# Performance work log

Hardware: AMD Instinct MI355X
Metric: run time of the kernel (lower is better)

## Reference

```python
import jax, jax.numpy as jnp
import numpy as np
from jax import lax

BN_EPS = 1e-5


def _conv_bn_relu(x, W, b, gamma, beta):
    # x: [B, Cin, N]; W: [Cout, Cin]; 1x1 conv == channel GEMM
    y = jnp.einsum('oc,bcn->bon', W, x) + b[None, :, None]
    mean = jnp.mean(y, axis=(0, 2), keepdims=True)
    var = jnp.mean((y - mean) ** 2, axis=(0, 2), keepdims=True)  # biased, torch BN train mode
    y = gamma[None, :, None] * (y - mean) / jnp.sqrt(var + BN_EPS) + beta[None, :, None]
    return jax.nn.relu(y)


def setup_inputs() -> dict:
    key = jax.random.key(0)
    ks = jax.random.split(key, 8)
    B, N1, N2, C1, C2 = 16, 4096, 1024, 128, 256
    Cin, H = C1 + C2, 256  # MLP dims [384, 256, 256]
    inp = {
        'centroids1': jax.random.normal(ks[0], (B, 3, N1), jnp.float32),
        'centroids2': jax.random.normal(ks[1], (B, 3, N2), jnp.float32),
        'features1': jax.random.normal(ks[2], (B, C1, N1), jnp.float32),
        'features2': jax.random.normal(ks[3], (B, C2, N2), jnp.float32),
        'W1': jax.random.normal(ks[4], (H, Cin), jnp.float32) / np.sqrt(Cin),
        'b1': jnp.zeros((H,), jnp.float32),
        'g1': jnp.ones((H,), jnp.float32),
        'be1': jnp.zeros((H,), jnp.float32),
        'W2': jax.random.normal(ks[5], (H, H), jnp.float32) / np.sqrt(H),
        'b2': jnp.zeros((H,), jnp.float32),
        'g2': jnp.ones((H,), jnp.float32),
        'be2': jnp.zeros((H,), jnp.float32),
    }
    return inp


def reference(centroids1, centroids2, features1, features2,
              W1, b1, g1, be1, W2, b2, g2, be2):
    c1 = centroids1.transpose(0, 2, 1)  # [B, N1, 3]
    c2 = centroids2.transpose(0, 2, 1)  # [B, N2, 3]
    f2 = features2.transpose(0, 2, 1)   # [B, N2, C2]

    # pairwise squared distances [B, N1, N2]
    d = (jnp.sum(c1 ** 2, -1)[:, :, None] + jnp.sum(c2 ** 2, -1)[:, None, :]
         - 2.0 * jnp.einsum('bnd,bmd->bnm', c1, c2))

    # 3 nearest neighbors (smallest distances)
    neg_top, idx = lax.top_k(-d, 3)            # idx: [B, N1, 3]
    dist3 = -neg_top
    recip = 1.0 / (dist3 + 1e-8)
    weight = recip / jnp.sum(recip, axis=2, keepdims=True)  # [B, N1, 3]

    gathered = jax.vmap(lambda f, i: f[i])(f2, idx)         # [B, N1, 3, C2]
    interp = jnp.sum(gathered * weight[..., None], axis=2)  # [B, N1, C2]

    feats = jnp.concatenate((features1.transpose(0, 2, 1), interp), axis=-1)  # [B, N1, C1+C2]
    x = feats.transpose(0, 2, 1)  # [B, C1+C2, N1]
    x = _conv_bn_relu(x, W1, b1, g1, be1)
    x = _conv_bn_relu(x, W2, b2, g2, be2)
    return x  # [B, 256, N1]
```

## Files before the change

### kernel.cpp

```cpp
#include <hip/hip_runtime.h>
#include <math.h>

#define N1 4096
#define N2 1024
#define C1 128
#define C2 256
#define CIN 384
#define H 256
#define BATCH 16
#define BN_EPS 1e-5f

typedef __attribute__((ext_vector_type(8))) short bf16x8;
typedef __attribute__((ext_vector_type(4))) float f32x4;

__device__ inline float bf2f(short s) {
    union { unsigned u; float f; } x;
    x.u = ((unsigned)(unsigned short)s) << 16;
    return x.f;
}
__device__ inline short f2bf(float f) {
    union { float f; unsigned u; } x; x.f = f;
    unsigned r = x.u + 0x7fffu + ((x.u >> 16) & 1u);
    return (short)(r >> 16);
}

__global__ __launch_bounds__(256)
void knn_kernel(const float* __restrict__ c1, const float* __restrict__ c2,
                float4* __restrict__ pk) {
    __shared__ __align__(16) float4 sc[N2];
    __shared__ float md[64 * 13];
    __shared__ int   mi[64 * 13];
    const int b = blockIdx.y;
    const float* c2b = c2 + (size_t)b * 3 * N2;
    for (int j = threadIdx.x; j < N2; j += 256) {
        float xx = c2b[j], yy = c2b[N2 + j], zz = c2b[2 * N2 + j];
        sc[j] = make_float4(xx, yy, zz, xx * xx + yy * yy + zz * zz);
    }
    __syncthreads();

    const int t = threadIdx.x;
    const int q = t & 63;
    const int quarter = t >> 6;
    const int n = blockIdx.x * 64 + q;
    const float* c1b = c1 + (size_t)b * 3 * N1;
    const float x = c1b[n], y = c1b[N1 + n], z = c1b[2 * N1 + n];
    const float s1 = x * x + y * y + z * z;

    float d0 = 3.4e38f, d1 = 3.4e38f, d2 = 3.4e38f;
    int i0 = 0, i1 = 0, i2 = 0;
    const int j0 = quarter * 256;
    #pragma unroll 8
    for (int jj = 0; jj < 256; ++jj) {
        const int j = j0 + jj;
        float4 cc = sc[j];
        float dot = x * cc.x + y * cc.y + z * cc.z;
        float d = s1 + cc.w - 2.0f * dot;
        bool c0v = d < d0, c1v = d < d1, c2v = d < d2;
        i2 = c1v ? i1 : (c2v ? j : i2);
        i1 = c0v ? i0 : (c1v ? j : i1);
        i0 = c0v ? j  : i0;
        d2 = __builtin_amdgcn_fmed3f(d1, d2, d);
        d1 = __builtin_amdgcn_fmed3f(d0, d1, d);
        d0 = fminf(d0, d);
    }
    const int mb = q * 13 + quarter * 3;
    md[mb + 0] = d0; md[mb + 1] = d1; md[mb + 2] = d2;
    mi[mb + 0] = i0; mi[mb + 1] = i1; mi[mb + 2] = i2;
    __syncthreads();

    if (t < 64) {
        float e0 = 3.4e38f, e1 = 3.4e38f, e2 = 3.4e38f;
        int a0 = 0, a1 = 0, a2 = 0;
        #pragma unroll
        for (int r = 0; r < 12; ++r) {
            const int rr = t * 13 + (r / 3) * 3 + (r % 3);
            float d = md[rr]; int j = mi[rr];
            bool c0 = d < e0, c1v = d < e1, c2v = d < e2;
            e2 = c1v ? e1 : (c2v ? d : e2);  a2 = c1v ? a1 : (c2v ? j : a2);
            e1 = c0 ? e0 : (c1v ? d : e1);   a1 = c0 ? a0 : (c1v ? j : a1);
            e0 = c0 ? d  : e0;               a0 = c0 ? j  : a0;
        }
        float r0 = 1.0f / (e0 + 1e-8f);
        float r1 = 1.0f / (e1 + 1e-8f);
        float r2 = 1.0f / (e2 + 1e-8f);
        float rs = r0 + r1 + r2;
        unsigned pack = (unsigned)a0 | ((unsigned)a1 << 10) | ((unsigned)a2 << 20);
        pk[(size_t)b * N1 + n] = make_float4(__uint_as_float(pack), r0 / rs, r1 / rs, r2 / rs);
    }
}

__global__ __launch_bounds__(256)
void prep_w(const float* __restrict__ W, short* __restrict__ Wsw, int K) {
    const int nkb = K >> 3;
    const int id = blockIdx.x * 256 + threadIdx.x;
    if (id >= 256 * nkb) return;
    const int m = id / nkb, kb = id % nkb;
    const float* src = W + (size_t)m * K + kb * 8;
    bf16x8 v;
    #pragma unroll
    for (int j = 0; j < 8; ++j) v[j] = f2bf(src[j]);
    *(bf16x8*)(Wsw + ((size_t)kb * 256 + m) * 8) = v;
}

__global__ __launch_bounds__(256)
void transpose_f2(const float* __restrict__ f2, short* __restrict__ f2t) {
    __shared__ float st[32][33];
    const int j0 = blockIdx.x * 32, c0 = blockIdx.y * 32, b = blockIdx.z;
    const int t = threadIdx.x;
    {
        const int cc = t >> 3, jj = (t & 7) * 4;
        const float* src = f2 + ((size_t)b * C2 + c0 + cc) * N2 + j0 + jj;
        float4 v = *(const float4*)src;
        st[cc][jj + 0] = v.x; st[cc][jj + 1] = v.y;
        st[cc][jj + 2] = v.z; st[cc][jj + 3] = v.w;
    }
    __syncthreads();
    {
        const int j = t >> 3, cb = (t & 7) * 4;
        short4 v = { f2bf(st[cb + 0][j]), f2bf(st[cb + 1][j]),
                     f2bf(st[cb + 2][j]), f2bf(st[cb + 3][j]) };
        *(short4*)(f2t + ((size_t)b * N2 + j0 + j) * C2 + c0 + cb) = v;
    }
}

__global__ __launch_bounds__(256)
void prep_B1(const short* __restrict__ f2t, const float4* __restrict__ pk,
             short* __restrict__ B1) {
    const int b = blockIdx.y;
    const int n = blockIdx.x * 256 + threadIdx.x;
    float4 v = pk[(size_t)b * N1 + n];
    unsigned u = __float_as_uint(v.x);
    const short* r0 = f2t + ((size_t)b * N2 + (u & 1023u)) * C2;
    const short* r1 = f2t + ((size_t)b * N2 + ((u >> 10) & 1023u)) * C2;
    const short* r2 = f2t + ((size_t)b * N2 + ((u >> 20) & 1023u)) * C2;
    short* ob = B1 + ((size_t)b * 32 * N1 + n) * 8;
    #pragma unroll 4
    for (int kb = 0; kb < 32; ++kb) {
        bf16x8 g0 = *(const bf16x8*)(r0 + kb * 8);
        bf16x8 g1 = *(const bf16x8*)(r1 + kb * 8);
        bf16x8 g2 = *(const bf16x8*)(r2 + kb * 8);
        bf16x8 o;
        #pragma unroll
        for (int e = 0; e < 8; ++e)
            o[e] = f2bf(fmaf(v.w, bf2f(g2[e]), fmaf(v.z, bf2f(g1[e]), v.y * bf2f(g0[e]))));
        *(bf16x8*)(ob + (size_t)kb * N1 * 8) = o;
    }
}

template<int MODE>
__global__ __launch_bounds__(256, 4)
void gemm_kernel(const short* __restrict__ Wsw,
                 const float* __restrict__ f1, const short* __restrict__ Bkc,
                 const float* __restrict__ scale, const float* __restrict__ shift,
                 short* __restrict__ Ykc, float2* __restrict__ P) {
    __shared__ float sc_s[256], sh_s[256];
    __shared__ float2 pb[128][2];

    const int t = threadIdx.x;
    const int d = blockIdx.x;
    const int grp = d >> 4, rem = d & 15;
    const int mh = rem >> 3;
    const int pair = grp * 8 + (rem & 7);
    const int nt = pair & 31, b = pair >> 5;
    const int n0 = nt * 128;

    const int lane = t & 63, wv = t >> 6;
    const int wm = wv >> 1, wn = wv & 1;
    const int l16 = lane & 15, lq = lane >> 4;

    if (MODE == 1) {
        sc_s[t] = scale[t]; sh_s[t] = shift[t];
        __syncthreads();
    }

    const short* Bb = Bkc + (size_t)b * 32 * N1 * 8;
    const short* Abase = Wsw + ((size_t)lq * 256 + mh * 128 + wm * 64 + l16) * 8;
    const int nfr = n0 + wn * 64 + l16;

    f32x4 acc[4][4];
    #pragma unroll
    for (int i = 0; i < 4; ++i)
        #pragma unroll
        for (int j = 0; j < 4; ++j)
            acc[i][j] = (f32x4){0.f, 0.f, 0.f, 0.f};

    if (MODE == 0) {
        const float* f1b = f1 + (size_t)b * C1 * N1;
        #pragma unroll
        for (int s = 0; s < 4; ++s) {
            bf16x8 a[4], bv[4];
            const short* ap = Abase + (size_t)s * 4 * 256 * 8;
            #pragma unroll
            for (int f = 0; f < 4; ++f) a[f] = *(const bf16x8*)(ap + f * 16 * 8);
            const float* fp = f1b + (size_t)(s * 32 + lq * 8) * N1 + nfr;
            #pragma unroll
            for (int f = 0; f < 4; ++f) {
                #pragma unroll
                for (int e = 0; e < 8; ++e)
                    bv[f][e] = f2bf(fp[(size_t)e * N1 + f * 16]);
            }
            #pragma unroll
            for (int i = 0; i < 4; ++i)
                #pragma unroll
                for (int j = 0; j < 4; ++j)
                    acc[i][j] = __builtin_amdgcn_mfma_f32_16x16x32_bf16(a[i], bv[j], acc[i][j], 0, 0, 0);
        }
        #pragma unroll
        for (int s = 4; s < 12; ++s) {
            bf16x8 a[4], bv[4];
            const short* ap = Abase + (size_t)s * 4 * 256 * 8;
            #pragma unroll
            for (int f = 0; f < 4; ++f) a[f] = *(const bf16x8*)(ap + f * 16 * 8);
            const short* bp = Bb + ((size_t)(s * 4 + lq - 16) * N1 + nfr) * 8;
            #pragma unroll
            for (int f = 0; f < 4; ++f) bv[f] = *(const bf16x8*)(bp + f * 16 * 8);
            #pragma unroll
            for (int i = 0; i < 4; ++i)
                #pragma unroll
                for (int j = 0; j < 4; ++j)
                    acc[i][j] = __builtin_amdgcn_mfma_f32_16x16x32_bf16(a[i], bv[j], acc[i][j], 0, 0, 0);
        }
    } else {
        #pragma unroll
        for (int s = 0; s < 8; ++s) {
            bf16x8 a[4], raw[4], bv[4];
            const short* ap = Abase + (size_t)s * 4 * 256 * 8;
            #pragma unroll
            for (int f = 0; f < 4; ++f) a[f] = *(const bf16x8*)(ap + f * 16 * 8);
            const short* bp = Bb + ((size_t)(s * 4 + lq) * N1 + nfr) * 8;
            #pragma unroll
            for (int f = 0; f < 4; ++f) raw[f] = *(const bf16x8*)(bp + f * 16 * 8);
            const int k0 = s * 32 + lq * 8;
            float sck[8], shk[8];
            #pragma unroll
            for (int e = 0; e < 8; ++e) { sck[e] = sc_s[k0 + e]; shk[e] = sh_s[k0 + e]; }
            #pragma unroll
            for (int f = 0; f < 4; ++f)
                #pragma unroll
                for (int e = 0; e < 8; ++e)
                    bv[f][e] = f2bf(fmaxf(fmaf(bf2f(raw[f][e]), sck[e], shk[e]), 0.f));
            #pragma unroll
            for (int i = 0; i < 4; ++i)
                #pragma unroll
                for (int j = 0; j < 4; ++j)
                    acc[i][j] = __builtin_amdgcn_mfma_f32_16x16x32_bf16(a[i], bv[j], acc[i][j], 0, 0, 0);
        }
    }

    short* Yb = Ykc + (size_t)b * 32 * N1 * 8;
    #pragma unroll
    for (int i = 0; i < 4; ++i) {
        const int kb = mh * 16 + wm * 8 + i * 2 + (lq >> 1);
        const int kr0 = (lq & 1) * 4;
        #pragma unroll
        for (int j = 0; j < 4; ++j) {
            const int n = n0 + wn * 64 + j * 16 + l16;
            short4 v = { f2bf(acc[i][j][0]), f2bf(acc[i][j][1]),
                         f2bf(acc[i][j][2]), f2bf(acc[i][j][3]) };
            *(short4*)(Yb + ((size_t)kb * N1 + n) * 8 + kr0) = v;
        }
    }

    #pragma unroll
    for (int i = 0; i < 4; ++i) {
        #pragma unroll
        for (int r = 0; r < 4; ++r) {
            float s = 0.f, qq = 0.f;
            #pragma unroll
            for (int j = 0; j < 4; ++j) {
                float xv = acc[i][j][r];
                s += xv; qq += xv * xv;
            }
            #pragma unroll
            for (int msk = 1; msk < 16; msk <<= 1) {
                s  += __shfl_xor(s, msk);
                qq += __shfl_xor(qq, msk);
            }
            if (l16 == 0)
                pb[wm * 64 + i * 16 + lq * 4 + r][wn] = make_float2(s, qq);
        }
    }
    __syncthreads();
    if (t < 128) {
        float2 a = pb[t][0], c = pb[t][1];
        P[(size_t)(mh * 128 + t) * 512 + b * 32 + nt] = make_float2(a.x + c.x, a.y + c.y);
    }
}

__global__ __launch_bounds__(256)
void bn_reduce(const float2* __restrict__ P, const float* __restrict__ g,
               const float* __restrict__ be, float* __restrict__ scale,
               float* __restrict__ shift) {
    const int c = blockIdx.x, t = threadIdx.x;
    float2 v0 = P[(size_t)c * 512 + t];
    float2 v1 = P[(size_t)c * 512 + 256 + t];
    float s = v0.x + v1.x, q = v0.y + v1.y;
    __shared__ float ss[256], sq[256];
    ss[t] = s; sq[t] = q;
    __syncthreads();
    for (int o = 128; o > 0; o >>= 1) {
        if (t < o) { ss[t] += ss[t + o]; sq[t] += sq[t + o]; }
        __syncthreads();
    }
    if (t == 0) {
        const float inv = 1.0f / (float)(BATCH * N1);
        float mean = ss[0] * inv;
        float var  = sq[0] * inv - mean * mean;
        float sc = g[c] / sqrtf(var + BN_EPS);
        scale[c] = sc;
        shift[c] = be[c] - mean * sc;
    }
}

__global__ __launch_bounds__(256)
void final_bn_relu(const short* __restrict__ y2kc, const float* __restrict__ scale,
                   const float* __restrict__ shift, float* __restrict__ out) {
    const int t = threadIdx.x;
    const int n0 = blockIdx.x * 1024 + t * 4;
    const int kb = blockIdx.y, b = blockIdx.z;
    const short* src = y2kc + ((size_t)(b * 32 + kb) * N1 + n0) * 8;
    bf16x8 v0 = *(const bf16x8*)(src);
    bf16x8 v1 = *(const bf16x8*)(src + 8);
    bf16x8 v2 = *(const bf16x8*)(src + 16);
    bf16x8 v3 = *(const bf16x8*)(src + 24);
    #pragma unroll
    for (int e = 0; e < 8; ++e) {
        const float sc = scale[kb * 8 + e], sh = shift[kb * 8 + e];
        float4 o;
        o.x = fmaxf(fmaf(bf2f(v0[e]), sc, sh), 0.f);
        o.y = fmaxf(fmaf(bf2f(v1[e]), sc, sh), 0.f);
        o.z = fmaxf(fmaf(bf2f(v2[e]), sc, sh), 0.f);
        o.w = fmaxf(fmaf(bf2f(v3[e]), sc, sh), 0.f);
        *(float4*)(out + ((size_t)(b * 256 + kb * 8 + e) * N1) + n0) = o;
    }
}

extern "C" void kernel_launch(void* const* d_in, const int* in_sizes, int n_in,
                              void* d_out, int out_size, void* d_ws, size_t ws_size,
                              hipStream_t stream) {
    const float* c1  = (const float*)d_in[0];
    const float* c2  = (const float*)d_in[1];
    const float* f1  = (const float*)d_in[2];
    const float* f2  = (const float*)d_in[3];
    const float* W1  = (const float*)d_in[4];
    const float* g1  = (const float*)d_in[6];
    const float* be1 = (const float*)d_in[7];
    const float* W2  = (const float*)d_in[8];
    const float* g2  = (const float*)d_in[10];
    const float* be2 = (const float*)d_in[11];
    float* out = (float*)d_out;

    char* ws = (char*)d_ws;
    short*  B1   = (short*)ws;
    short*  y2kc = (short*)ws;
    short*  f2t  = (short*)(ws + (32u << 20));
    short*  y1kc = (short*)(ws + (32u << 20));
    short*  W1s  = (short*)(ws + (64u << 20));
    short*  W2s  = (short*)(ws + (64u << 20) + (256u << 10));
    float4* pk   = (float4*)(ws + (64u << 20) + (512u << 10));
    float2* P    = (float2*)(ws + (64u << 20) + (512u << 10) + (1u << 20));
    float* scale1 = (float*)(ws + (64u << 20) + (512u << 10) + (2u << 20));
    float* shift1 = scale1 + 256;
    float* scale2 = shift1 + 256;
    float* shift2 = scale2 + 256;

    prep_w<<<48, 256, 0, stream>>>(W1, W1s, CIN);
    prep_w<<<32, 256, 0, stream>>>(W2, W2s, H);
    transpose_f2<<<dim3(N2 / 32, C2 / 32, BATCH), 256, 0, stream>>>(f2, f2t);
    knn_kernel<<<dim3(N1 / 64, BATCH), 256, 0, stream>>>(c1, c2, pk);
    prep_B1<<<dim3(N1 / 256, BATCH), 256, 0, stream>>>(f2t, pk, B1);

    gemm_kernel<0><<<1024, 256, 0, stream>>>(
        W1s, f1, B1, nullptr, nullptr, y1kc, P);
    bn_reduce<<<256, 256, 0, stream>>>(P, g1, be1, scale1, shift1);

    gemm_kernel<1><<<1024, 256, 0, stream>>>(
        W2s, nullptr, y1kc, scale1, shift1, y2kc, P);
    bn_reduce<<<256, 256, 0, stream>>>(P, g2, be2, scale2, shift2);

    final_bn_relu<<<dim3(N1 / 1024, 32, BATCH), 256, 0, stream>>>(y2kc, scale2, shift2, out);
}
```

Before: 151.4 us.

## Restage GEMM tiles through LDS with full-M blocks and prune KNN updates

Each GEMM block now covers all 256 output channels for 64 points and stages its whole B tile in LDS once, using global_load_lds. Layer-1 features are converted to bf16 straight into shared memory, and the M-half split and the partial-stat reduction in LDS are gone. BN partial sums are written per block, so bn_reduce now sums four partials per thread. The KNN kernel folds the -2 factor and |c1|^2 out of the inner loop and skips the top-3 insertion when no lane in the wavefront improves, which adds wave-level branching in exchange for fewer selects.

```diff
diff --git a/kernel.cpp b/kernel.cpp
--- a/kernel.cpp
+++ b/kernel.cpp
@@ -22,6 +22,12 @@
     union { float f; unsigned u; } x; x.f = f;
     unsigned r = x.u + 0x7fffu + ((x.u >> 16) & 1u);
     return (short)(r >> 16);
+}
+
+typedef const __attribute__((address_space(1))) unsigned int guint;
+typedef __attribute__((address_space(3))) unsigned int luint;
+__device__ inline void gll16(const void* g, void* l) {
+    __builtin_amdgcn_global_load_lds((guint*)g, (luint*)l, 16, 0, 0);
 }
 
 __global__ __launch_bounds__(256)
@@ -34,7 +40,7 @@
     const float* c2b = c2 + (size_t)b * 3 * N2;
     for (int j = threadIdx.x; j < N2; j += 256) {
         float xx = c2b[j], yy = c2b[N2 + j], zz = c2b[2 * N2 + j];
-        sc[j] = make_float4(xx, yy, zz, xx * xx + yy * yy + zz * zz);
+        sc[j] = make_float4(-2.f * xx, -2.f * yy, -2.f * zz, xx * xx + yy * yy + zz * zz);
     }
     __syncthreads();
 
@@ -44,24 +50,25 @@
     const int n = blockIdx.x * 64 + q;
     const float* c1b = c1 + (size_t)b * 3 * N1;
     const float x = c1b[n], y = c1b[N1 + n], z = c1b[2 * N1 + n];
-    const float s1 = x * x + y * y + z * z;
 
     float d0 = 3.4e38f, d1 = 3.4e38f, d2 = 3.4e38f;
     int i0 = 0, i1 = 0, i2 = 0;
     const int j0 = quarter * 256;
-    #pragma unroll 8
+    #pragma unroll 4
     for (int jj = 0; jj < 256; ++jj) {
         const int j = j0 + jj;
         float4 cc = sc[j];
-        float dot = x * cc.x + y * cc.y + z * cc.z;
-        float d = s1 + cc.w - 2.0f * dot;
-        bool c0v = d < d0, c1v = d < d1, c2v = d < d2;
-        i2 = c1v ? i1 : (c2v ? j : i2);
-        i1 = c0v ? i0 : (c1v ? j : i1);
-        i0 = c0v ? j  : i0;
-        d2 = __builtin_amdgcn_fmed3f(d1, d2, d);
-        d1 = __builtin_amdgcn_fmed3f(d0, d1, d);
-        d0 = fminf(d0, d);
+        float d = fmaf(x, cc.x, fmaf(y, cc.y, fmaf(z, cc.z, cc.w)));
+        bool c2v = d < d2;
+        if (__any(c2v)) {
+            bool c0v = d < d0, c1v = d < d1;
+            i2 = c1v ? i1 : (c2v ? j : i2);
+            i1 = c0v ? i0 : (c1v ? j : i1);
+            i0 = c0v ? j  : i0;
+            d2 = __builtin_amdgcn_fmed3f(d1, d2, d);
+            d1 = __builtin_amdgcn_fmed3f(d0, d1, d);
+            d0 = fminf(d0, d);
+        }
     }
     const int mb = q * 13 + quarter * 3;
     md[mb + 0] = d0; md[mb + 1] = d1; md[mb + 2] = d2;
@@ -80,9 +87,10 @@
             e1 = c0 ? e0 : (c1v ? d : e1);   a1 = c0 ? a0 : (c1v ? j : a1);
             e0 = c0 ? d  : e0;               a0 = c0 ? j  : a0;
         }
-        float r0 = 1.0f / (e0 + 1e-8f);
-        float r1 = 1.0f / (e1 + 1e-8f);
-        float r2 = 1.0f / (e2 + 1e-8f);
+        const float s1 = x * x + y * y + z * z;
+        float r0 = 1.0f / (e0 + s1 + 1e-8f);
+        float r1 = 1.0f / (e1 + s1 + 1e-8f);
+        float r2 = 1.0f / (e2 + s1 + 1e-8f);
         float rs = r0 + r1 + r2;
         unsigned pack = (unsigned)a0 | ((unsigned)a1 << 10) | ((unsigned)a2 << 20);
         pk[(size_t)b * N1 + n] = make_float4(__uint_as_float(pack), r0 / rs, r1 / rs, r2 / rs);
@@ -147,35 +155,59 @@
     }
 }
 
-template<int MODE>
-__global__ __launch_bounds__(256, 4)
+template<int NT, bool BN>
+__global__ __launch_bounds__(256)
 void gemm_kernel(const short* __restrict__ Wsw,
                  const float* __restrict__ f1, const short* __restrict__ Bkc,
                  const float* __restrict__ scale, const float* __restrict__ shift,
                  short* __restrict__ Ykc, float2* __restrict__ P) {
+    constexpr bool M0 = (NT == 12);
+
+    __shared__ __align__(16) short B_lds[4 * NT][64][8];
     __shared__ float sc_s[256], sh_s[256];
-    __shared__ float2 pb[128][2];
 
     const int t = threadIdx.x;
-    const int d = blockIdx.x;
-    const int grp = d >> 4, rem = d & 15;
-    const int mh = rem >> 3;
-    const int pair = grp * 8 + (rem & 7);
-    const int nt = pair & 31, b = pair >> 5;
-    const int n0 = nt * 128;
+    const int blk = blockIdx.x;
+    const int b = blk >> 6, nt = blk & 63;
+    const int n0 = nt * 64;
 
     const int lane = t & 63, wv = t >> 6;
-    const int wm = wv >> 1, wn = wv & 1;
+    const int wm = wv;
     const int l16 = lane & 15, lq = lane >> 4;
 
-    if (MODE == 1) {
-        sc_s[t] = scale[t]; sh_s[t] = shift[t];
-        __syncthreads();
-    }
+    if (BN) { sc_s[t] = scale[t]; sh_s[t] = shift[t]; }
 
     const short* Bb = Bkc + (size_t)b * 32 * N1 * 8;
-    const short* Abase = Wsw + ((size_t)lq * 256 + mh * 128 + wm * 64 + l16) * 8;
-    const int nfr = n0 + wn * 64 + l16;
+
+    #pragma unroll
+    for (int i = 0; i < 8; ++i) {
+        const int u = wv * 8 + i;
+        const int dst_kb = M0 ? (16 + u) : u;
+        const short* g = Bb + ((size_t)u * N1 + n0 + lane) * 8;
+        gll16(g, &B_lds[dst_kb][0][0]);
+    }
+    if (M0) {
+        const float* f1b = f1 + (size_t)b * C1 * N1;
+        const int kbt = t >> 4, nq = (t & 15) * 4;
+        float4 fv[8];
+        #pragma unroll
+        for (int e = 0; e < 8; ++e)
+            fv[e] = *(const float4*)(f1b + (size_t)(kbt * 8 + e) * N1 + n0 + nq);
+        #pragma unroll
+        for (int j = 0; j < 4; ++j) {
+            bf16x8 pv;
+            pv[0] = f2bf(j == 0 ? fv[0].x : j == 1 ? fv[0].y : j == 2 ? fv[0].z : fv[0].w);
+            pv[1] = f2bf(j == 0 ? fv[1].x : j == 1 ? fv[1].y : j == 2 ? fv[1].z : fv[1].w);
+            pv[2] = f2bf(j == 0 ? fv[2].x : j == 1 ? fv[2].y : j == 2 ? fv[2].z : fv[2].w);
+            pv[3] = f2bf(j == 0 ? fv[3].x : j == 1 ? fv[3].y : j == 2 ? fv[3].z : fv[3].w);
+            pv[4] = f2bf(j == 0 ? fv[4].x : j == 1 ? fv[4].y : j == 2 ? fv[4].z : fv[4].w);
+            pv[5] = f2bf(j == 0 ? fv[5].x : j == 1 ? fv[5].y : j == 2 ? fv[5].z : fv[5].w);
+            pv[6] = f2bf(j == 0 ? fv[6].x : j == 1 ? fv[6].y : j == 2 ? fv[6].z : fv[6].w);
+            pv[7] = f2bf(j == 0 ? fv[7].x : j == 1 ? fv[7].y : j == 2 ? fv[7].z : fv[7].w);
+            *(bf16x8*)&B_lds[kbt][nq + j][0] = pv;
+        }
+    }
+    __syncthreads();
 
     f32x4 acc[4][4];
     #pragma unroll
@@ -184,77 +216,45 @@
         for (int j = 0; j < 4; ++j)
             acc[i][j] = (f32x4){0.f, 0.f, 0.f, 0.f};
 
-    if (MODE == 0) {
-        const float* f1b = f1 + (size_t)b * C1 * N1;
-        #pragma unroll
-        for (int s = 0; s < 4; ++s) {
-            bf16x8 a[4], bv[4];
-            const short* ap = Abase + (size_t)s * 4 * 256 * 8;
-            #pragma unroll
-            for (int f = 0; f < 4; ++f) a[f] = *(const bf16x8*)(ap + f * 16 * 8);
-            const float* fp = f1b + (size_t)(s * 32 + lq * 8) * N1 + nfr;
+    #pragma unroll
+    for (int s = 0; s < NT; ++s) {
+        bf16x8 a[4], bb4[4];
+        const short* ap = Wsw + ((size_t)(s * 4 + lq) * 256 + wm * 64 + l16) * 8;
+        #pragma unroll
+        for (int f = 0; f < 4; ++f)
+            a[f] = *(const bf16x8*)(ap + (size_t)f * 16 * 8);
+        if (BN) {
+            const int k0 = s * 32 + lq * 8;
+            float sck[8], shk[8];
+            #pragma unroll
+            for (int e = 0; e < 8; ++e) { sck[e] = sc_s[k0 + e]; shk[e] = sh_s[k0 + e]; }
             #pragma unroll
             for (int f = 0; f < 4; ++f) {
+                bf16x8 raw = *(const bf16x8*)&B_lds[s * 4 + lq][f * 16 + l16][0];
                 #pragma unroll
                 for (int e = 0; e < 8; ++e)
-                    bv[f][e] = f2bf(fp[(size_t)e * N1 + f * 16]);
+                    bb4[f][e] = f2bf(fmaxf(fmaf(bf2f(raw[e]), sck[e], shk[e]), 0.f));
             }
-            #pragma unroll
-            for (int i = 0; i < 4; ++i)
-                #pragma unroll
-                for (int j = 0; j < 4; ++j)
-                    acc[i][j] = __builtin_amdgcn_mfma_f32_16x16x32_bf16(a[i], bv[j], acc[i][j], 0, 0, 0);
-        }
-        #pragma unroll
-        for (int s = 4; s < 12; ++s) {
-            bf16x8 a[4], bv[4];
-            const short* ap = Abase + (size_t)s * 4 * 256 * 8;
-            #pragma unroll
-            for (int f = 0; f < 4; ++f) a[f] = *(const bf16x8*)(ap + f * 16 * 8);
-            const short* bp = Bb + ((size_t)(s * 4 + lq - 16) * N1 + nfr) * 8;
-            #pragma unroll
-            for (int f = 0; f < 4; ++f) bv[f] = *(const bf16x8*)(bp + f * 16 * 8);
-            #pragma unroll
-            for (int i = 0; i < 4; ++i)
-                #pragma unroll
-                for (int j = 0; j < 4; ++j)
-                    acc[i][j] = __builtin_amdgcn_mfma_f32_16x16x32_bf16(a[i], bv[j], acc[i][j], 0, 0, 0);
-        }
-    } else {
-        #pragma unroll
-        for (int s = 0; s < 8; ++s) {
-            bf16x8 a[4], raw[4], bv[4];
-            const short* ap = Abase + (size_t)s * 4 * 256 * 8;
-            #pragma unroll
-            for (int f = 0; f < 4; ++f) a[f] = *(const bf16x8*)(ap + f * 16 * 8);
-            const short* bp = Bb + ((size_t)(s * 4 + lq) * N1 + nfr) * 8;
-            #pragma unroll
-            for (int f = 0; f < 4; ++f) raw[f] = *(const bf16x8*)(bp + f * 16 * 8);
-            const int k0 = s * 32 + lq * 8;
-            float sck[8], shk[8];
-            #pragma unroll
-            for (int e = 0; e < 8; ++e) { sck[e] = sc_s[k0 + e]; shk[e] = sh_s[k0 + e]; }
+        } else {
             #pragma unroll
             for (int f = 0; f < 4; ++f)
-                #pragma unroll
-                for (int e = 0; e < 8; ++e)
-                    bv[f][e] = f2bf(fmaxf(fmaf(bf2f(raw[f][e]), sck[e], shk[e]), 0.f));
-            #pragma unroll
-            for (int i = 0; i < 4; ++i)
-                #pragma unroll
-                for (int j = 0; j < 4; ++j)
-                    acc[i][j] = __builtin_amdgcn_mfma_f32_16x16x32_bf16(a[i], bv[j], acc[i][j], 0, 0, 0);
-        }
+                bb4[f] = *(const bf16x8*)&B_lds[s * 4 + lq][f * 16 + l16][0];
+        }
+        #pragma unroll
+        for (int i = 0; i < 4; ++i)
+            #pragma unroll
+            for (int j = 0; j < 4; ++j)
+                acc[i][j] = __builtin_amdgcn_mfma_f32_16x16x32_bf16(a[i], bb4[j], acc[i][j], 0, 0, 0);
     }
 
     short* Yb = Ykc + (size_t)b * 32 * N1 * 8;
     #pragma unroll
     for (int i = 0; i < 4; ++i) {
-        const int kb = mh * 16 + wm * 8 + i * 2 + (lq >> 1);
+        const int kb = wm * 8 + i * 2 + (lq >> 1);
         const int kr0 = (lq & 1) * 4;
         #pragma unroll
         for (int j = 0; j < 4; ++j) {
-            const int n = n0 + wn * 64 + j * 16 + l16;
+            const int n = n0 + j * 16 + l16;
             short4 v = { f2bf(acc[i][j][0]), f2bf(acc[i][j][1]),
                          f2bf(acc[i][j][2]), f2bf(acc[i][j][3]) };
             *(short4*)(Yb + ((size_t)kb * N1 + n) * 8 + kr0) = v;
@@ -276,14 +276,11 @@
                 s  += __shfl_xor(s, msk);
                 qq += __shfl_xor(qq, msk);
             }
-            if (l16 == 0)
-                pb[wm * 64 + i * 16 + lq * 4 + r][wn] = make_float2(s, qq);
-        }
-    }
-    __syncthreads();
-    if (t < 128) {
-        float2 a = pb[t][0], c = pb[t][1];
-        P[(size_t)(mh * 128 + t) * 512 + b * 32 + nt] = make_float2(a.x + c.x, a.y + c.y);
+            if (l16 == 0) {
+                const int c = wm * 64 + i * 16 + lq * 4 + r;
+                P[(size_t)c * 1024 + blk] = make_float2(s, qq);
+            }
+        }
     }
 }
 
@@ -292,9 +289,12 @@
                const float* __restrict__ be, float* __restrict__ scale,
                float* __restrict__ shift) {
     const int c = blockIdx.x, t = threadIdx.x;
-    float2 v0 = P[(size_t)c * 512 + t];
-    float2 v1 = P[(size_t)c * 512 + 256 + t];
-    float s = v0.x + v1.x, q = v0.y + v1.y;
+    float s = 0.f, q = 0.f;
+    #pragma unroll
+    for (int r = 0; r < 4; ++r) {
+        float2 v = P[(size_t)c * 1024 + r * 256 + t];
+        s += v.x; q += v.y;
+    }
     __shared__ float ss[256], sq[256];
     ss[t] = s; sq[t] = q;
     __syncthreads();
@@ -358,8 +358,8 @@
     short*  W1s  = (short*)(ws + (64u << 20));
     short*  W2s  = (short*)(ws + (64u << 20) + (256u << 10));
     float4* pk   = (float4*)(ws + (64u << 20) + (512u << 10));
-    float2* P    = (float2*)(ws + (64u << 20) + (512u << 10) + (1u << 20));
-    float* scale1 = (float*)(ws + (64u << 20) + (512u << 10) + (2u << 20));
+    float2* P    = (float2*)(ws + (64u << 20) + (1536u << 10));
+    float* scale1 = (float*)(ws + (64u << 20) + (3584u << 10));
     float* shift1 = scale1 + 256;
     float* scale2 = shift1 + 256;
     float* shift2 = scale2 + 256;
@@ -370,11 +370,11 @@
     knn_kernel<<<dim3(N1 / 64, BATCH), 256, 0, stream>>>(c1, c2, pk);
     prep_B1<<<dim3(N1 / 256, BATCH), 256, 0, stream>>>(f2t, pk, B1);
 
-    gemm_kernel<0><<<1024, 256, 0, stream>>>(
+    gemm_kernel<12, false><<<1024, 256, 0, stream>>>(
         W1s, f1, B1, nullptr, nullptr, y1kc, P);
     bn_reduce<<<256, 256, 0, stream>>>(P, g1, be1, scale1, shift1);
 
-    gemm_kernel<1><<<1024, 256, 0, stream>>>(
+    gemm_kernel<8, true><<<1024, 256, 0, stream>>>(
         W2s, nullptr, y1kc, scale1, shift1, y2kc, P);
     bn_reduce<<<256, 256, 0, stream>>>(P, g2, be2, scale2, shift2);
 
```

Result: slower. 160.7 us (+6.1%).
